# Optimization experiments

Hardware: AMD Instinct MI355X
Metric: run time of the kernel (lower is better)

Reference implementation:

```python
import jax, jax.numpy as jnp
import numpy as np

VOCAB = 50257
D_MODEL = 768
N_LAYERS = 4
N_HEADS = 12
D_HEAD = D_MODEL // N_HEADS
MAX_LEN = 5000
EPS = 1e-5


def _make_pe(max_len, d_model):
    # sinusoidal PE, interleaved sin/cos, base n=10000 (matches PositionalEncodingLayer)
    pos = jnp.arange(max_len, dtype=jnp.float32)[:, None]            # [L,1]
    i = jnp.arange(d_model // 2, dtype=jnp.float32)[None, :]         # [1,D/2]
    theta = pos / jnp.power(10000.0, 2.0 * i / d_model)              # [L,D/2]
    pe = jnp.zeros((max_len, d_model), dtype=jnp.float32)
    pe = pe.at[:, 0::2].set(jnp.sin(theta))
    pe = pe.at[:, 1::2].set(jnp.cos(theta))
    return pe


def setup_inputs() -> dict:
    key = jax.random.key(0)
    ks = jax.random.split(key, 10)
    B, S = 2, 1024
    tokens = jax.random.randint(ks[0], (B, S), 0, VOCAB)
    std = 0.02
    embed = jax.random.normal(ks[1], (VOCAB, D_MODEL), jnp.float32) * std
    pe = _make_pe(MAX_LEN, D_MODEL)
    # per-layer stacked params, torch nn.Linear convention: y = x @ W.T + b
    wq_w = jax.random.normal(ks[2], (N_LAYERS, D_MODEL, D_MODEL), jnp.float32) * std
    wk_w = jax.random.normal(ks[3], (N_LAYERS, D_MODEL, D_MODEL), jnp.float32) * std
    wv_w = jax.random.normal(ks[4], (N_LAYERS, D_MODEL, D_MODEL), jnp.float32) * std
    lin_w = jax.random.normal(ks[5], (N_LAYERS, D_MODEL, D_MODEL), jnp.float32) * std
    wq_b = jnp.zeros((N_LAYERS, D_MODEL), jnp.float32)
    wk_b = jnp.zeros((N_LAYERS, D_MODEL), jnp.float32)
    wv_b = jnp.zeros((N_LAYERS, D_MODEL), jnp.float32)
    lin_b = jnp.zeros((N_LAYERS, D_MODEL), jnp.float32)
    n1_s = jnp.ones((N_LAYERS, D_MODEL), jnp.float32)
    n1_b = jnp.zeros((N_LAYERS, D_MODEL), jnp.float32)
    n2_s = jnp.ones((N_LAYERS, D_MODEL), jnp.float32)
    n2_b = jnp.zeros((N_LAYERS, D_MODEL), jnp.float32)
    unembed_w = jax.random.normal(ks[6], (VOCAB, D_MODEL), jnp.float32) * std
    unembed_b = jnp.zeros((VOCAB,), jnp.float32)
    return dict(tokens=tokens, embed=embed, pe=pe,
                wq_w=wq_w, wq_b=wq_b, wk_w=wk_w, wk_b=wk_b, wv_w=wv_w, wv_b=wv_b,
                lin_w=lin_w, lin_b=lin_b, n1_s=n1_s, n1_b=n1_b, n2_s=n2_s, n2_b=n2_b,
                unembed_w=unembed_w, unembed_b=unembed_b)


def _layernorm(x, scale, bias):
    m = jnp.mean(x, axis=-1, keepdims=True)
    v = jnp.mean(jnp.square(x - m), axis=-1, keepdims=True)
    return (x - m) * jax.lax.rsqrt(v + EPS) * scale + bias


def _attn_block(x, wq_w, wq_b, wk_w, wk_b, wv_w, wv_b, lin_w, lin_b, n1_s, n1_b, n2_s, n2_b):
    B, S, D = x.shape
    def proj(w, b):
        y = x @ w.T + b
        return y.reshape(B, S, N_HEADS, D_HEAD).transpose(0, 2, 1, 3)  # [B,H,S,Dh]
    q, k, v = proj(wq_w, wq_b), proj(wk_w, wk_b), proj(wv_w, wv_b)
    scores = jnp.einsum('bhqd,bhkd->bhqk', q, k) / jnp.sqrt(jnp.float32(D_HEAD))
    causal = jnp.tril(jnp.ones((S, S), dtype=bool))
    scores = jnp.where(causal, scores, -jnp.inf)
    probs = jax.nn.softmax(scores, axis=-1)
    attn = jnp.einsum('bhqk,bhkd->bhqd', probs, v)
    attn = attn.transpose(0, 2, 1, 3).reshape(B, S, D)
    x = _layernorm(x + attn, n1_s, n1_b)
    x = _layernorm(x + (x @ lin_w.T + lin_b), n2_s, n2_b)
    return x


def reference(tokens, embed, pe, wq_w, wq_b, wk_w, wk_b, wv_w, wv_b,
              lin_w, lin_b, n1_s, n1_b, n2_s, n2_b, unembed_w, unembed_b):
    B, S = tokens.shape
    x = embed[tokens] + pe[:S]
    for l in range(N_LAYERS):
        x = _attn_block(x, wq_w[l], wq_b[l], wk_w[l], wk_b[l], wv_w[l], wv_b[l],
                        lin_w[l], lin_b[l], n1_s[l], n1_b[l], n2_s[l], n2_b[l])
    logits = x @ unembed_w.T + unembed_b
    return logits
```

## Files before the change

### kernel.cpp

```cpp
#include <hip/hip_runtime.h>
#include <hip/hip_bf16.h>


#define VOCAB 50257
#define DM 768
#define NL 4
#define NH 12
#define DH 64
#define SEQ 1024
#define BATCH 2
#define ROWS (BATCH * SEQ)

typedef __attribute__((ext_vector_type(8))) short short8;
typedef __attribute__((ext_vector_type(4))) float f32x4;

__device__ __forceinline__ unsigned short f2bf(float f) {
    union { float f; unsigned u; } v; v.f = f;
    unsigned r = v.u + 0x7FFFu + ((v.u >> 16) & 1u);
    return (unsigned short)(r >> 16);
}

__global__ __launch_bounds__(256) void cvt_kernel(const float* __restrict__ in,
                                                  unsigned short* __restrict__ out,
                                                  int n4) {
    int i = blockIdx.x * 256 + threadIdx.x;
    if (i < n4) {
        float4 v = ((const float4*)in)[i];
        ushort4 o;
        o.x = f2bf(v.x); o.y = f2bf(v.y); o.z = f2bf(v.z); o.w = f2bf(v.w);
        ((ushort4*)out)[i] = o;
    }
}

__global__ __launch_bounds__(256) void embed_kernel(const int* __restrict__ tok,
                                                    const float* __restrict__ emb,
                                                    const float* __restrict__ pe,
                                                    float* __restrict__ xf,
                                                    unsigned short* __restrict__ xb) {
    int row = blockIdx.x;
    int t = tok[row];
    int s = row & (SEQ - 1);
    #pragma unroll
    for (int j = 0; j < 3; ++j) {
        int c = threadIdx.x + j * 256;
        float v = emb[(size_t)t * DM + c] + pe[(size_t)s * DM + c];
        xf[(size_t)row * DM + c] = v;
        xb[(size_t)row * DM + c] = f2bf(v);
    }
}

__device__ __forceinline__ float block_sum(float x, float* red) {
    #pragma unroll
    for (int off = 32; off > 0; off >>= 1) x += __shfl_down(x, off);
    int w = threadIdx.x >> 6;
    if ((threadIdx.x & 63) == 0) red[w] = x;
    __syncthreads();
    float t = (red[0] + red[1]) + (red[2] + red[3]);
    __syncthreads();
    return t;
}

__global__ __launch_bounds__(256) void ln_kernel(const float* __restrict__ A,
                                                 const float* __restrict__ Bi,
                                                 const float* __restrict__ sc,
                                                 const float* __restrict__ bi,
                                                 float* __restrict__ xf,
                                                 unsigned short* __restrict__ xb) {
    __shared__ float red[4];
    int row = blockIdx.x, tid = threadIdx.x;
    const float* ap = A + (size_t)row * DM;
    const float* bp = Bi + (size_t)row * DM;
    float v[3], sum = 0.f;
    #pragma unroll
    for (int j = 0; j < 3; ++j) { v[j] = ap[tid + j * 256] + bp[tid + j * 256]; sum += v[j]; }
    sum = block_sum(sum, red);
    float mean = sum * (1.f / DM);
    float vs = 0.f;
    #pragma unroll
    for (int j = 0; j < 3; ++j) { float d = v[j] - mean; vs += d * d; }
    vs = block_sum(vs, red);
    float rstd = rsqrtf(vs * (1.f / DM) + 1e-5f);
    #pragma unroll
    for (int j = 0; j < 3; ++j) {
        int c = tid + j * 256;
        float o = (v[j] - mean) * rstd * sc[c] + bi[c];
        xf[(size_t)row * DM + c] = o;
        xb[(size_t)row * DM + c] = f2bf(o);
    }
}

template <int OUT_BF16>
__global__ __launch_bounds__(256) void gemm_bt(const unsigned short* __restrict__ A, int lda,
                                               const unsigned short* __restrict__ B, int ldb,
                                               const float* __restrict__ bias,
                                               void* __restrict__ C, int ldc,
                                               int M, int N, int K) {
    __shared__ __align__(16) unsigned short As[64 * 64];
    __shared__ __align__(16) unsigned short Bs[64 * 64];
    const int tid = threadIdx.x;
    const int m0 = blockIdx.x * 64;
    const int n0 = blockIdx.y * 64;
    const int lane = tid & 63, wid = tid >> 6;
    const int wm = wid >> 1, wn = wid & 1;
    const int lr = lane & 15, lq = lane >> 4;
    const int srow = tid >> 3;
    const int scol = (tid & 7) * 8;
    f32x4 acc[2][2] = {};

    for (int k0 = 0; k0 < K; k0 += 64) {
        #pragma unroll
        for (int r = 0; r < 2; ++r) {
            int row = r * 32 + srow;
            {
                const unsigned short* src = A + (size_t)(m0 + row) * lda + k0 + scol;
                short8 v = *reinterpret_cast<const short8*>(src);
                *reinterpret_cast<short8*>(&As[(row * 64 + scol) ^ ((row & 7) << 3)]) = v;
            }
            {
                int brow = n0 + row; if (brow >= N) brow = N - 1;
                const unsigned short* src = B + (size_t)brow * ldb + k0 + scol;
                short8 v = *reinterpret_cast<const short8*>(src);
                *reinterpret_cast<short8*>(&Bs[(row * 64 + scol) ^ ((row & 7) << 3)]) = v;
            }
        }
        __syncthreads();
        #pragma unroll
        for (int kk = 0; kk < 2; ++kk) {
            short8 a[2], b[2];
            int kc = kk * 32 + lq * 8;
            #pragma unroll
            for (int i = 0; i < 2; ++i) {
                int ar = wm * 32 + i * 16 + lr;
                a[i] = *reinterpret_cast<const short8*>(&As[(ar * 64 + kc) ^ ((ar & 7) << 3)]);
                int br = wn * 32 + i * 16 + lr;
                b[i] = *reinterpret_cast<const short8*>(&Bs[(br * 64 + kc) ^ ((br & 7) << 3)]);
            }
            #pragma unroll
            for (int i = 0; i < 2; ++i)
                #pragma unroll
                for (int j = 0; j < 2; ++j)
                    acc[i][j] = __builtin_amdgcn_mfma_f32_16x16x32_bf16(a[i], b[j], acc[i][j], 0, 0, 0);
        }
        __syncthreads();
    }
    #pragma unroll
    for (int i = 0; i < 2; ++i) {
        int row = m0 + wm * 32 + i * 16 + lq * 4;
        #pragma unroll
        for (int j = 0; j < 2; ++j) {
            int col = n0 + wn * 32 + j * 16 + lr;
            if (col < N) {
                float bv = bias[col];
                #pragma unroll
                for (int r = 0; r < 4; ++r) {
                    float v = acc[i][j][r] + bv;
                    if (OUT_BF16) ((unsigned short*)C)[(size_t)(row + r) * ldc + col] = f2bf(v);
                    else          ((float*)C)[(size_t)(row + r) * ldc + col] = v;
                }
            }
        }
    }
}

__global__ __launch_bounds__(256) void attn_kernel(const unsigned short* __restrict__ Q,
                                                   const unsigned short* __restrict__ K,
                                                   const unsigned short* __restrict__ V,
                                                   float* __restrict__ O) {
    __shared__ __align__(16) unsigned short Ks[64 * 64];
    __shared__ __align__(16) unsigned short Vs[64 * 64];
    __shared__ __align__(16) unsigned short Ps[4][16 * 64];
    const int qb = blockIdx.x;
    const int bh = blockIdx.y;
    const int b = bh / NH, h = bh % NH;
    const int tid = threadIdx.x, lane = tid & 63, w = tid >> 6;
    const int lr = lane & 15, lq = lane >> 4;
    const int wq0 = qb * 64 + w * 16;
    const size_t base = (size_t)b * SEQ * DM + h * DH;

    short8 qf[2];
    {
        const unsigned short* qp = Q + base + (size_t)(wq0 + lr) * DM + lq * 8;
        qf[0] = *reinterpret_cast<const short8*>(qp);
        qf[1] = *reinterpret_cast<const short8*>(qp + 32);
    }
    f32x4 o_acc[4] = {};
    float mrow[4], lrow[4];
    #pragma unroll
    for (int r = 0; r < 4; ++r) { mrow[r] = -1e30f; lrow[r] = 0.f; }

    const int srow = tid >> 3, scol = (tid & 7) * 8;
    for (int t = 0; t <= qb; ++t) {
        const int kv0 = t * 64;
        #pragma unroll
        for (int rr = 0; rr < 2; ++rr) {
            int row = rr * 32 + srow;
            {
                const unsigned short* kp = K + base + (size_t)(kv0 + row) * DM + scol;
                short8 v = *reinterpret_cast<const short8*>(kp);
                *reinterpret_cast<short8*>(&Ks[(row * 64 + scol) ^ ((row & 7) << 3)]) = v;
            }
            {
                const unsigned short* vp = V + base + (size_t)(kv0 + row) * DM + scol;
                short8 v = *reinterpret_cast<const short8*>(vp);
                #pragma unroll
                for (int j = 0; j < 8; ++j) {
                    int d = scol + j;
                    Vs[(d * 64 + row) ^ ((d & 7) << 3)] = (unsigned short)v[j];
                }
            }
        }
        __syncthreads();
        if (kv0 <= wq0 + 15) {
            f32x4 s[4];
            #pragma unroll
            for (int n = 0; n < 4; ++n) {
                int br = n * 16 + lr;
                short8 b0 = *reinterpret_cast<const short8*>(&Ks[(br * 64 + lq * 8) ^ ((br & 7) << 3)]);
                short8 b1 = *reinterpret_cast<const short8*>(&Ks[(br * 64 + 32 + lq * 8) ^ ((br & 7) << 3)]);
                f32x4 z = {};
                z = __builtin_amdgcn_mfma_f32_16x16x32_bf16(qf[0], b0, z, 0, 0, 0);
                z = __builtin_amdgcn_mfma_f32_16x16x32_bf16(qf[1], b1, z, 0, 0, 0);
                s[n] = z;
            }
            const bool diag = (t == qb);
            #pragma unroll
            for (int n = 0; n < 4; ++n)
                #pragma unroll
                for (int r = 0; r < 4; ++r) {
                    float v = s[n][r] * 0.125f;
                    if (diag) {
                        int rg = wq0 + lq * 4 + r;
                        int cg = kv0 + n * 16 + lr;
                        if (cg > rg) v = -1e30f;
                    }
                    s[n][r] = v;
                }
            float f[4];
            #pragma unroll
            for (int r = 0; r < 4; ++r) {
                float mx = fmaxf(fmaxf(s[0][r], s[1][r]), fmaxf(s[2][r], s[3][r]));
                #pragma unroll
                for (int off = 1; off < 16; off <<= 1) mx = fmaxf(mx, __shfl_xor(mx, off));
                float mn = fmaxf(mrow[r], mx);
                f[r] = exp2f((mrow[r] - mn) * 1.44269504f);
                mrow[r] = mn;
            }
            #pragma unroll
            for (int n = 0; n < 4; ++n)
                #pragma unroll
                for (int r = 0; r < 4; ++r)
                    s[n][r] = exp2f((s[n][r] - mrow[r]) * 1.44269504f);
            #pragma unroll
            for (int r = 0; r < 4; ++r) {
                float ls = ((s[0][r] + s[1][r]) + (s[2][r] + s[3][r]));
                #pragma unroll
                for (int off = 1; off < 16; off <<= 1) ls += __shfl_xor(ls, off);
                lrow[r] = lrow[r] * f[r] + ls;
            }
            #pragma unroll
            for (int n = 0; n < 4; ++n)
                #pragma unroll
                for (int r = 0; r < 4; ++r) {
                    int pr = lq * 4 + r, pc = n * 16 + lr;
                    Ps[w][(pr * 64 + pc) ^ ((pr & 7) << 3)] = f2bf(s[n][r]);
                }
            #pragma unroll
            for (int n = 0; n < 4; ++n)
                #pragma unroll
                for (int r = 0; r < 4; ++r) o_acc[n][r] *= f[r];
            #pragma unroll
            for (int kk = 0; kk < 2; ++kk) {
                short8 pa = *reinterpret_cast<const short8*>(
                    &Ps[w][(lr * 64 + kk * 32 + lq * 8) ^ ((lr & 7) << 3)]);
                #pragma unroll
                for (int n = 0; n < 4; ++n) {
                    int vr = n * 16 + lr;
                    short8 bv = *reinterpret_cast<const short8*>(
                        &Vs[(vr * 64 + kk * 32 + lq * 8) ^ ((vr & 7) << 3)]);
                    o_acc[n] = __builtin_amdgcn_mfma_f32_16x16x32_bf16(pa, bv, o_acc[n], 0, 0, 0);
                }
            }
        }
        __syncthreads();
    }
    #pragma unroll
    for (int r = 0; r < 4; ++r) {
        float inv = 1.f / lrow[r];
        int row = wq0 + lq * 4 + r;
        #pragma unroll
        for (int n = 0; n < 4; ++n)
            O[base + (size_t)row * DM + n * 16 + lr] = o_acc[n][r] * inv;
    }
}

extern "C" void kernel_launch(void* const* d_in, const int* in_sizes, int n_in,
                              void* d_out, int out_size, void* d_ws, size_t ws_size,
                              hipStream_t stream) {
    const int*   tokens   = (const int*)d_in[0];
    const float* embed    = (const float*)d_in[1];
    const float* pe       = (const float*)d_in[2];
    const float* wq_w     = (const float*)d_in[3];
    const float* wq_b     = (const float*)d_in[4];
    const float* wk_w     = (const float*)d_in[5];
    const float* wk_b     = (const float*)d_in[6];
    const float* wv_w     = (const float*)d_in[7];
    const float* wv_b     = (const float*)d_in[8];
    const float* lin_w    = (const float*)d_in[9];
    const float* lin_b    = (const float*)d_in[10];
    const float* n1_s     = (const float*)d_in[11];
    const float* n1_b     = (const float*)d_in[12];
    const float* n2_s     = (const float*)d_in[13];
    const float* n2_b     = (const float*)d_in[14];
    const float* unemb_w  = (const float*)d_in[15];
    const float* unemb_b  = (const float*)d_in[16];

    char* ws = (char*)d_ws;
    size_t off = 0;
    auto carve = [&](size_t bytes) { char* p = ws + off; off += (bytes + 255) & ~(size_t)255; return p; };
    float*          xf    = (float*)carve((size_t)ROWS * DM * 4);
    float*          attn  = (float*)carve((size_t)ROWS * DM * 4);
    float*          yb    = (float*)carve((size_t)ROWS * DM * 4);
    unsigned short* xb    = (unsigned short*)carve((size_t)ROWS * DM * 2);
    unsigned short* qb_   = (unsigned short*)carve((size_t)ROWS * DM * 2);
    unsigned short* kb_   = (unsigned short*)carve((size_t)ROWS * DM * 2);
    unsigned short* vb_   = (unsigned short*)carve((size_t)ROWS * DM * 2);
    unsigned short* wq_h  = (unsigned short*)carve((size_t)NL * DM * DM * 2);
    unsigned short* wk_h  = (unsigned short*)carve((size_t)NL * DM * DM * 2);
    unsigned short* wv_h  = (unsigned short*)carve((size_t)NL * DM * DM * 2);
    unsigned short* lin_h = (unsigned short*)carve((size_t)NL * DM * DM * 2);
    unsigned short* ue_h  = (unsigned short*)carve((size_t)VOCAB * DM * 2);

    {
        int nw4 = NL * DM * DM / 4;
        cvt_kernel<<<(nw4 + 255) / 256, 256, 0, stream>>>(wq_w, wq_h, nw4);
        cvt_kernel<<<(nw4 + 255) / 256, 256, 0, stream>>>(wk_w, wk_h, nw4);
        cvt_kernel<<<(nw4 + 255) / 256, 256, 0, stream>>>(wv_w, wv_h, nw4);
        cvt_kernel<<<(nw4 + 255) / 256, 256, 0, stream>>>(lin_w, lin_h, nw4);
        int nu4 = VOCAB * DM / 4;
        cvt_kernel<<<(nu4 + 255) / 256, 256, 0, stream>>>(unemb_w, ue_h, nu4);
    }
    embed_kernel<<<ROWS, 256, 0, stream>>>(tokens, embed, pe, xf, xb);

    for (int l = 0; l < NL; ++l) {
        const size_t wo = (size_t)l * DM * DM;
        gemm_bt<1><<<dim3(ROWS / 64, DM / 64), 256, 0, stream>>>(
            xb, DM, wq_h + wo, DM, wq_b + l * DM, qb_, DM, ROWS, DM, DM);
        gemm_bt<1><<<dim3(ROWS / 64, DM / 64), 256, 0, stream>>>(
            xb, DM, wk_h + wo, DM, wk_b + l * DM, kb_, DM, ROWS, DM, DM);
        gemm_bt<1><<<dim3(ROWS / 64, DM / 64), 256, 0, stream>>>(
            xb, DM, wv_h + wo, DM, wv_b + l * DM, vb_, DM, ROWS, DM, DM);
        attn_kernel<<<dim3(SEQ / 64, BATCH * NH), 256, 0, stream>>>(qb_, kb_, vb_, attn);
        ln_kernel<<<ROWS, 256, 0, stream>>>(xf, attn, n1_s + l * DM, n1_b + l * DM, xf, xb);
        gemm_bt<0><<<dim3(ROWS / 64, DM / 64), 256, 0, stream>>>(
            xb, DM, lin_h + wo, DM, lin_b + l * DM, yb, DM, ROWS, DM, DM);
        ln_kernel<<<ROWS, 256, 0, stream>>>(xf, yb, n2_s + l * DM, n2_b + l * DM, xf, xb);
    }
    gemm_bt<0><<<dim3(ROWS / 64, (VOCAB + 63) / 64), 256, 0, stream>>>(
        xb, DM, ue_h, DM, unemb_b, (float*)d_out, VOCAB, ROWS, VOCAB, DM);
}
```

Measured before the change: 884.4 us.

## Fuse QKV projections into one GEMM and enlarge GEMM tiles to 128x128

Concatenates the Q, K and V weights and biases so that each layer runs one GEMM producing a packed QKV buffer, which the attention kernel reads with a stride. The GEMM tile grows from 64x64 to 128x128, global-to-LDS direct loads replace register staging, and the block index is remapped with an XCD-aware swizzle. This is meant to cut launches and raise data reuse per tile, especially in the large unembedding GEMM. The larger tile leaves the 768-wide layer GEMMs with fewer blocks, and it uses more registers.

Result: faster. 809.3 us (-8.5%).

```diff
diff --git a/kernel.cpp b/kernel.cpp
--- a/kernel.cpp
+++ b/kernel.cpp
@@ -10,6 +10,7 @@
 #define SEQ 1024
 #define BATCH 2
 #define ROWS (BATCH * SEQ)
+#define QKVN (3 * DM)
 
 typedef __attribute__((ext_vector_type(8))) short short8;
 typedef __attribute__((ext_vector_type(4))) float f32x4;
@@ -19,6 +20,11 @@
     unsigned r = v.u + 0x7FFFu + ((v.u >> 16) & 1u);
     return (unsigned short)(r >> 16);
 }
+
+#define GLOAD16(gp, lp)                                                        \
+    __builtin_amdgcn_global_load_lds(                                          \
+        (const __attribute__((address_space(1))) unsigned int*)(gp),           \
+        (__attribute__((address_space(3))) unsigned int*)(lp), 16, 0, 0)
 
 __global__ __launch_bounds__(256) void cvt_kernel(const float* __restrict__ in,
                                                   unsigned short* __restrict__ out,
@@ -30,6 +36,37 @@
         o.x = f2bf(v.x); o.y = f2bf(v.y); o.z = f2bf(v.z); o.w = f2bf(v.w);
         ((ushort4*)out)[i] = o;
     }
+}
+
+__global__ __launch_bounds__(256) void cvt_qkv_kernel(const float* __restrict__ wq,
+                                                      const float* __restrict__ wk,
+                                                      const float* __restrict__ wv,
+                                                      unsigned short* __restrict__ dst,
+                                                      int n4) {
+    int i = blockIdx.x * 256 + threadIdx.x;
+    if (i >= n4) return;
+    const int PER_L = 3 * DM * DM / 4, PER_W = DM * DM / 4;
+    int l = i / PER_L;
+    int rem = i - l * PER_L;
+    int w = rem / PER_W;
+    int r2 = rem - w * PER_W;
+    const float* src = (w == 0) ? wq : (w == 1) ? wk : wv;
+    float4 v = ((const float4*)src)[(size_t)l * PER_W + r2];
+    ushort4 o;
+    o.x = f2bf(v.x); o.y = f2bf(v.y); o.z = f2bf(v.z); o.w = f2bf(v.w);
+    ((ushort4*)dst)[i] = o;
+}
+
+__global__ __launch_bounds__(256) void pack_qkv_bias(const float* __restrict__ bq,
+                                                     const float* __restrict__ bk,
+                                                     const float* __restrict__ bv,
+                                                     float* __restrict__ dst) {
+    int i = blockIdx.x * 256 + threadIdx.x;
+    if (i >= NL * QKVN) return;
+    int l = i / QKVN, c = i - l * QKVN;
+    int w = c / DM, cc = c - w * DM;
+    const float* src = (w == 0) ? bq : (w == 1) ? bk : bv;
+    dst[i] = src[l * DM + cc];
 }
 
 __global__ __launch_bounds__(256) void embed_kernel(const int* __restrict__ tok,
@@ -90,72 +127,83 @@
 }
 
 template <int OUT_BF16>
-__global__ __launch_bounds__(256) void gemm_bt(const unsigned short* __restrict__ A, int lda,
-                                               const unsigned short* __restrict__ B, int ldb,
+__global__ __launch_bounds__(256) void gemm128(const unsigned short* __restrict__ A,
+                                               const unsigned short* __restrict__ B,
                                                const float* __restrict__ bias,
-                                               void* __restrict__ C, int ldc,
-                                               int M, int N, int K) {
-    __shared__ __align__(16) unsigned short As[64 * 64];
-    __shared__ __align__(16) unsigned short Bs[64 * 64];
-    const int tid = threadIdx.x;
-    const int m0 = blockIdx.x * 64;
-    const int n0 = blockIdx.y * 64;
-    const int lane = tid & 63, wid = tid >> 6;
+                                               void* __restrict__ C,
+                                               int M, int N, int K, int gx) {
+    __shared__ __align__(16) unsigned short As[128 * 64];
+    __shared__ __align__(16) unsigned short Bs[128 * 64];
+    int bid = blockIdx.x;
+    const int nwg = gridDim.x;
+    if ((nwg & 7) == 0) {
+        int q = nwg >> 3;
+        bid = (bid & 7) * q + (bid >> 3);
+    }
+    const int bx = bid % gx, by = bid / gx;
+    const int m0 = bx * 128, n0 = by * 128;
+    const int tid = threadIdx.x, lane = tid & 63, wid = tid >> 6;
     const int wm = wid >> 1, wn = wid & 1;
     const int lr = lane & 15, lq = lane >> 4;
-    const int srow = tid >> 3;
-    const int scol = (tid & 7) * 8;
-    f32x4 acc[2][2] = {};
+
+    const int sr = wid * 32 + (lane >> 3);
+    const int sch = lane & 7;
+    const int scs = sch ^ (sr & 7);
+    const unsigned short* aP[4];
+    const unsigned short* bP[4];
+    unsigned short* aL[4];
+    unsigned short* bL[4];
+    #pragma unroll
+    for (int i = 0; i < 4; ++i) {
+        int r = sr + i * 8;
+        aP[i] = A + (size_t)(m0 + r) * K + scs * 8;
+        int br = n0 + r; if (br >= N) br = N - 1;
+        bP[i] = B + (size_t)br * K + scs * 8;
+        aL[i] = &As[r * 64 + sch * 8];
+        bL[i] = &Bs[r * 64 + sch * 8];
+    }
+
+    f32x4 acc[4][4] = {};
 
     for (int k0 = 0; k0 < K; k0 += 64) {
         #pragma unroll
-        for (int r = 0; r < 2; ++r) {
-            int row = r * 32 + srow;
-            {
-                const unsigned short* src = A + (size_t)(m0 + row) * lda + k0 + scol;
-                short8 v = *reinterpret_cast<const short8*>(src);
-                *reinterpret_cast<short8*>(&As[(row * 64 + scol) ^ ((row & 7) << 3)]) = v;
-            }
-            {
-                int brow = n0 + row; if (brow >= N) brow = N - 1;
-                const unsigned short* src = B + (size_t)brow * ldb + k0 + scol;
-                short8 v = *reinterpret_cast<const short8*>(src);
-                *reinterpret_cast<short8*>(&Bs[(row * 64 + scol) ^ ((row & 7) << 3)]) = v;
-            }
-        }
+        for (int i = 0; i < 4; ++i) GLOAD16(aP[i] + k0, aL[i]);
+        #pragma unroll
+        for (int i = 0; i < 4; ++i) GLOAD16(bP[i] + k0, bL[i]);
         __syncthreads();
         #pragma unroll
         for (int kk = 0; kk < 2; ++kk) {
-            short8 a[2], b[2];
-            int kc = kk * 32 + lq * 8;
-            #pragma unroll
-            for (int i = 0; i < 2; ++i) {
-                int ar = wm * 32 + i * 16 + lr;
-                a[i] = *reinterpret_cast<const short8*>(&As[(ar * 64 + kc) ^ ((ar & 7) << 3)]);
-                int br = wn * 32 + i * 16 + lr;
-                b[i] = *reinterpret_cast<const short8*>(&Bs[(br * 64 + kc) ^ ((br & 7) << 3)]);
-            }
-            #pragma unroll
-            for (int i = 0; i < 2; ++i)
-                #pragma unroll
-                for (int j = 0; j < 2; ++j)
+            short8 a[4], b[4];
+            #pragma unroll
+            for (int i = 0; i < 4; ++i) {
+                int ar = wm * 64 + i * 16 + lr;
+                a[i] = *reinterpret_cast<const short8*>(
+                    &As[ar * 64 + (((kk * 4 + lq) ^ (ar & 7)) * 8)]);
+                int br = wn * 64 + i * 16 + lr;
+                b[i] = *reinterpret_cast<const short8*>(
+                    &Bs[br * 64 + (((kk * 4 + lq) ^ (br & 7)) * 8)]);
+            }
+            #pragma unroll
+            for (int i = 0; i < 4; ++i)
+                #pragma unroll
+                for (int j = 0; j < 4; ++j)
                     acc[i][j] = __builtin_amdgcn_mfma_f32_16x16x32_bf16(a[i], b[j], acc[i][j], 0, 0, 0);
         }
         __syncthreads();
     }
     #pragma unroll
-    for (int i = 0; i < 2; ++i) {
-        int row = m0 + wm * 32 + i * 16 + lq * 4;
-        #pragma unroll
-        for (int j = 0; j < 2; ++j) {
-            int col = n0 + wn * 32 + j * 16 + lr;
+    for (int i = 0; i < 4; ++i) {
+        int row = m0 + wm * 64 + i * 16 + lq * 4;
+        #pragma unroll
+        for (int j = 0; j < 4; ++j) {
+            int col = n0 + wn * 64 + j * 16 + lr;
             if (col < N) {
                 float bv = bias[col];
                 #pragma unroll
                 for (int r = 0; r < 4; ++r) {
                     float v = acc[i][j][r] + bv;
-                    if (OUT_BF16) ((unsigned short*)C)[(size_t)(row + r) * ldc + col] = f2bf(v);
-                    else          ((float*)C)[(size_t)(row + r) * ldc + col] = v;
+                    if (OUT_BF16) ((unsigned short*)C)[(size_t)(row + r) * N + col] = f2bf(v);
+                    else          ((float*)C)[(size_t)(row + r) * N + col] = v;
                 }
             }
         }
@@ -165,6 +213,7 @@
 __global__ __launch_bounds__(256) void attn_kernel(const unsigned short* __restrict__ Q,
                                                    const unsigned short* __restrict__ K,
                                                    const unsigned short* __restrict__ V,
+                                                   int ld,
                                                    float* __restrict__ O) {
     __shared__ __align__(16) unsigned short Ks[64 * 64];
     __shared__ __align__(16) unsigned short Vs[64 * 64];
@@ -175,11 +224,12 @@
     const int tid = threadIdx.x, lane = tid & 63, w = tid >> 6;
     const int lr = lane & 15, lq = lane >> 4;
     const int wq0 = qb * 64 + w * 16;
-    const size_t base = (size_t)b * SEQ * DM + h * DH;
+    const size_t base = (size_t)b * SEQ * ld + h * DH;
+    const size_t obase = (size_t)b * SEQ * DM + h * DH;
 
     short8 qf[2];
     {
-        const unsigned short* qp = Q + base + (size_t)(wq0 + lr) * DM + lq * 8;
+        const unsigned short* qp = Q + base + (size_t)(wq0 + lr) * ld + lq * 8;
         qf[0] = *reinterpret_cast<const short8*>(qp);
         qf[1] = *reinterpret_cast<const short8*>(qp + 32);
     }
@@ -195,12 +245,12 @@
         for (int rr = 0; rr < 2; ++rr) {
             int row = rr * 32 + srow;
             {
-                const unsigned short* kp = K + base + (size_t)(kv0 + row) * DM + scol;
+                const unsigned short* kp = K + base + (size_t)(kv0 + row) * ld + scol;
                 short8 v = *reinterpret_cast<const short8*>(kp);
                 *reinterpret_cast<short8*>(&Ks[(row * 64 + scol) ^ ((row & 7) << 3)]) = v;
             }
             {
-                const unsigned short* vp = V + base + (size_t)(kv0 + row) * DM + scol;
+                const unsigned short* vp = V + base + (size_t)(kv0 + row) * ld + scol;
                 short8 v = *reinterpret_cast<const short8*>(vp);
                 #pragma unroll
                 for (int j = 0; j < 8; ++j) {
@@ -289,7 +339,7 @@
         int row = wq0 + lq * 4 + r;
         #pragma unroll
         for (int n = 0; n < 4; ++n)
-            O[base + (size_t)row * DM + n * 16 + lr] = o_acc[n][r] * inv;
+            O[obase + (size_t)row * DM + n * 16 + lr] = o_acc[n][r] * inv;
     }
 }
 
@@ -317,44 +367,40 @@
     char* ws = (char*)d_ws;
     size_t off = 0;
     auto carve = [&](size_t bytes) { char* p = ws + off; off += (bytes + 255) & ~(size_t)255; return p; };
-    float*          xf    = (float*)carve((size_t)ROWS * DM * 4);
-    float*          attn  = (float*)carve((size_t)ROWS * DM * 4);
-    float*          yb    = (float*)carve((size_t)ROWS * DM * 4);
-    unsigned short* xb    = (unsigned short*)carve((size_t)ROWS * DM * 2);
-    unsigned short* qb_   = (unsigned short*)carve((size_t)ROWS * DM * 2);
-    unsigned short* kb_   = (unsigned short*)carve((size_t)ROWS * DM * 2);
-    unsigned short* vb_   = (unsigned short*)carve((size_t)ROWS * DM * 2);
-    unsigned short* wq_h  = (unsigned short*)carve((size_t)NL * DM * DM * 2);
-    unsigned short* wk_h  = (unsigned short*)carve((size_t)NL * DM * DM * 2);
-    unsigned short* wv_h  = (unsigned short*)carve((size_t)NL * DM * DM * 2);
-    unsigned short* lin_h = (unsigned short*)carve((size_t)NL * DM * DM * 2);
-    unsigned short* ue_h  = (unsigned short*)carve((size_t)VOCAB * DM * 2);
+    float*          xf     = (float*)carve((size_t)ROWS * DM * 4);
+    float*          yb     = (float*)carve((size_t)ROWS * DM * 4);
+    unsigned short* xb     = (unsigned short*)carve((size_t)ROWS * DM * 2);
+    unsigned short* qkv    = (unsigned short*)carve((size_t)ROWS * QKVN * 2);
+    unsigned short* wqkv_h = (unsigned short*)carve((size_t)NL * QKVN * DM * 2);
+    unsigned short* lin_h  = (unsigned short*)carve((size_t)NL * DM * DM * 2);
+    unsigned short* ue_h   = (unsigned short*)carve((size_t)VOCAB * DM * 2);
+    float*          qkvb   = (float*)carve((size_t)NL * QKVN * 4);
 
     {
-        int nw4 = NL * DM * DM / 4;
-        cvt_kernel<<<(nw4 + 255) / 256, 256, 0, stream>>>(wq_w, wq_h, nw4);
-        cvt_kernel<<<(nw4 + 255) / 256, 256, 0, stream>>>(wk_w, wk_h, nw4);
-        cvt_kernel<<<(nw4 + 255) / 256, 256, 0, stream>>>(wv_w, wv_h, nw4);
-        cvt_kernel<<<(nw4 + 255) / 256, 256, 0, stream>>>(lin_w, lin_h, nw4);
+        int nq4 = NL * QKVN * DM / 4;
+        cvt_qkv_kernel<<<(nq4 + 255) / 256, 256, 0, stream>>>(wq_w, wk_w, wv_w, wqkv_h, nq4);
+        int nl4 = NL * DM * DM / 4;
+        cvt_kernel<<<(nl4 + 255) / 256, 256, 0, stream>>>(lin_w, lin_h, nl4);
         int nu4 = VOCAB * DM / 4;
         cvt_kernel<<<(nu4 + 255) / 256, 256, 0, stream>>>(unemb_w, ue_h, nu4);
+        pack_qkv_bias<<<(NL * QKVN + 255) / 256, 256, 0, stream>>>(wq_b, wk_b, wv_b, qkvb);
     }
     embed_kernel<<<ROWS, 256, 0, stream>>>(tokens, embed, pe, xf, xb);
 
+    const int gx = ROWS / 128;
     for (int l = 0; l < NL; ++l) {
-        const size_t wo = (size_t)l * DM * DM;
-        gemm_bt<1><<<dim3(ROWS / 64, DM / 64), 256, 0, stream>>>(
-            xb, DM, wq_h + wo, DM, wq_b + l * DM, qb_, DM, ROWS, DM, DM);
-        gemm_bt<1><<<dim3(ROWS / 64, DM / 64), 256, 0, stream>>>(
-            xb, DM, wk_h + wo, DM, wk_b + l * DM, kb_, DM, ROWS, DM, DM);
-        gemm_bt<1><<<dim3(ROWS / 64, DM / 64), 256, 0, stream>>>(
-            xb, DM, wv_h + wo, DM, wv_b + l * DM, vb_, DM, ROWS, DM, DM);
-        attn_kernel<<<dim3(SEQ / 64, BATCH * NH), 256, 0, stream>>>(qb_, kb_, vb_, attn);
-        ln_kernel<<<ROWS, 256, 0, stream>>>(xf, attn, n1_s + l * DM, n1_b + l * DM, xf, xb);
-        gemm_bt<0><<<dim3(ROWS / 64, DM / 64), 256, 0, stream>>>(
-            xb, DM, lin_h + wo, DM, lin_b + l * DM, yb, DM, ROWS, DM, DM);
+        gemm128<1><<<gx * (QKVN / 128), 256, 0, stream>>>(
+            xb, wqkv_h + (size_t)l * QKVN * DM, qkvb + l * QKVN, qkv,
+            ROWS, QKVN, DM, gx);
+        attn_kernel<<<dim3(SEQ / 64, BATCH * NH), 256, 0, stream>>>(
+            qkv, qkv + DM, qkv + 2 * DM, QKVN, yb);
+        ln_kernel<<<ROWS, 256, 0, stream>>>(xf, yb, n1_s + l * DM, n1_b + l * DM, xf, xb);
+        gemm128<0><<<gx * (DM / 128), 256, 0, stream>>>(
+            xb, lin_h + (size_t)l * DM * DM, lin_b + l * DM, yb,
+            ROWS, DM, DM, gx);
         ln_kernel<<<ROWS, 256, 0, stream>>>(xf, yb, n2_s + l * DM, n2_b + l * DM, xf, xb);
     }
-    gemm_bt<0><<<dim3(ROWS / 64, (VOCAB + 63) / 64), 256, 0, stream>>>(
-        xb, DM, ue_h, DM, unemb_b, (float*)d_out, VOCAB, ROWS, VOCAB, DM);
-}
+    const int gyu = (VOCAB + 127) / 128;
+    gemm128<0><<<gx * gyu, 256, 0, stream>>>(
+        xb, ue_h, unemb_b, (float*)d_out, ROWS, VOCAB, DM, gx);
+}
```
